# Optimization experiments

Measured on AMD Instinct MI355X. Metric: run time of the kernel, lower is better.

## Reference

```python
import jax, jax.numpy as jnp
import numpy as np

EMBED_DIM = 768
NUM_HEADS = 12
HEAD_DIM = EMBED_DIM // NUM_HEADS
SCALE = HEAD_DIM ** -0.5


def setup_inputs() -> dict:
    key = jax.random.key(0)
    ks = jax.random.split(key, 9)
    B, S, D = 2, 2048, EMBED_DIM
    init = 1.0 / np.sqrt(D)  # ~ nn.Linear default uniform scale
    x = jax.random.normal(ks[0], (B, S, D), dtype=jnp.float32)
    Wq = jax.random.uniform(ks[1], (D, D), jnp.float32, -init, init)
    bq = jax.random.uniform(ks[2], (D,), jnp.float32, -init, init)
    Wk = jax.random.uniform(ks[3], (D, D), jnp.float32, -init, init)
    bk = jax.random.uniform(ks[4], (D,), jnp.float32, -init, init)
    Wv = jax.random.uniform(ks[5], (D, D), jnp.float32, -init, init)
    bv = jax.random.uniform(ks[6], (D,), jnp.float32, -init, init)
    Wo = jax.random.uniform(ks[7], (D, D), jnp.float32, -init, init)
    bo = jax.random.uniform(ks[8], (D,), jnp.float32, -init, init)
    return {"x": x, "Wq": Wq, "bq": bq, "Wk": Wk, "bk": bk,
            "Wv": Wv, "bv": bv, "Wo": Wo, "bo": bo}


def reference(x, Wq, bq, Wk, bk, Wv, bv, Wo, bo):
    B, S, D = x.shape
    H, Dh = NUM_HEADS, HEAD_DIM
    # projections; weights stored as (in, out) so x @ W == torch Linear with W.T
    q = (x @ Wq + bq).reshape(B, S, H, Dh).transpose(0, 2, 1, 3)  # [B,H,S,Dh]
    k = (x @ Wk + bk).reshape(B, S, H, Dh).transpose(0, 2, 1, 3)
    v = (x @ Wv + bv).reshape(B, S, H, Dh).transpose(0, 2, 1, 3)
    scores = jnp.einsum("bhqd,bhkd->bhqk", q, k) * SCALE        # [B,H,S,S]
    weights = jax.nn.softmax(scores, axis=-1)
    out = jnp.einsum("bhqk,bhkd->bhqd", weights, v)              # [B,H,S,Dh]
    out = out.transpose(0, 2, 1, 3).reshape(B, S, D)
    return out @ Wo + bo
```

## Files before the change

kernel.cpp:

```cpp
#include <hip/hip_runtime.h>
#include <math.h>

#define BB 2
#define SS 2048
#define DDIM 768
#define HH 12
#define DH 64
#define NROWS (BB*SS)
#define NTOK_D (NROWS*DDIM)
#define NQT2 (SS/128)

typedef _Float16 f16;
typedef _Float16 half2v __attribute__((ext_vector_type(2)));
typedef __fp16 fp16x2 __attribute__((ext_vector_type(2)));
typedef _Float16 half4 __attribute__((ext_vector_type(4)));
typedef _Float16 half8 __attribute__((ext_vector_type(8)));
typedef float f32x4 __attribute__((ext_vector_type(4)));

__device__ __forceinline__ half2v cvt_pk_f16(float a, float b) {
    fp16x2 t = __builtin_amdgcn_cvt_pkrtz(a, b);
    return __builtin_bit_cast(half2v, t);
}

#define MFMA16(a,b,c) __builtin_amdgcn_mfma_f32_16x16x32_f16((a),(b),(c),0,0,0)
#define QSCALE (0.125f * 1.44269504088896f)
#define M_STATIC 10.0f

__device__ __forceinline__ int swz(int row, int chunk16) {
    return row*128 + ((chunk16 ^ (row & 7)) << 4);
}

__global__ __launch_bounds__(256) void prep_x(const float* __restrict__ x, f16* __restrict__ xh)
{
    int i = blockIdx.x * 256 + threadIdx.x;
    const float4* in = (const float4*)x;
    float4 a = in[i*2], b = in[i*2+1];
    half8 h = {(f16)a.x,(f16)a.y,(f16)a.z,(f16)a.w,(f16)b.x,(f16)b.y,(f16)b.z,(f16)b.w};
    *(half8*)(xh + (size_t)i*8) = h;
}

__global__ __launch_bounds__(256) void prep_w(const float* __restrict__ Wq, const float* __restrict__ Wk,
                                              const float* __restrict__ Wv, const float* __restrict__ Wo,
                                              f16* __restrict__ Wt)
{
    const int z = blockIdx.z;
    const float* W = z==0 ? Wq : (z==1 ? Wk : (z==2 ? Wv : Wo));
    f16* out = Wt + (size_t)z * DDIM * DDIM;

    __shared__ float tile[64][65];
    const int t = threadIdx.x;
    const int k0 = blockIdx.x*64, n0 = blockIdx.y*64;

    const int kr = t >> 2, nc = (t & 3) * 16;
    #pragma unroll
    for (int i = 0; i < 4; ++i) {
        float4 v = *(const float4*)&W[(size_t)(k0+kr)*DDIM + n0 + nc + i*4];
        tile[kr][nc+i*4+0] = v.x; tile[kr][nc+i*4+1] = v.y;
        tile[kr][nc+i*4+2] = v.z; tile[kr][nc+i*4+3] = v.w;
    }
    __syncthreads();
    const int nr = t >> 2, kc = (t & 3) * 16;
    half8 h0, h1;
    #pragma unroll
    for (int j = 0; j < 8; ++j) {
        h0[j] = (f16)tile[kc + j][nr];
        h1[j] = (f16)tile[kc + 8 + j][nr];
    }
    *(half8*)&out[(size_t)(n0+nr)*DDIM + k0 + kc]     = h0;
    *(half8*)&out[(size_t)(n0+nr)*DDIM + k0 + kc + 8] = h1;
}

__global__ __launch_bounds__(256) void proj_qkv(const f16* __restrict__ Xh, const f16* __restrict__ Wt,
        const float* __restrict__ bq, const float* __restrict__ bk, const float* __restrict__ bv,
        f16* __restrict__ qb, f16* __restrict__ kb2, f16* __restrict__ vtb)
{
    const int z = blockIdx.z;
    const f16* Wz = Wt + (size_t)z * DDIM * DDIM;
    const float* bias = z==0 ? bq : (z==1 ? bk : bv);
    const float qscale = (z==0) ? QSCALE : 1.0f;

    __shared__ __align__(16) unsigned char lds[64*1024];

    const int tid = threadIdx.x;
    const int l = tid & 63, w = tid >> 6;
    const int g = l >> 4, qi = l & 15;
    const int wm = w >> 1, wn = w & 1;
    const int m0 = blockIdx.x * 128, n0 = blockIdx.y * 128;

    f32x4 acc[4][4];
    #pragma unroll
    for (int i=0;i<4;i++)
        #pragma unroll
        for (int j=0;j<4;j++) { f32x4 zv = {0.f,0.f,0.f,0.f}; acc[i][j] = zv; }

    half8 sa[4], sb[4];

#define GLOAD(t) { \
        _Pragma("unroll") \
        for (int i = 0; i < 4; ++i) { \
            int c = i*256 + tid, row = c >> 3, kc = c & 7; \
            sa[i] = *(const half8*)&Xh[(size_t)(m0+row)*DDIM + (t)*64 + kc*8]; \
            sb[i] = *(const half8*)&Wz[(size_t)(n0+row)*DDIM + (t)*64 + kc*8]; \
        } }

#define GWRT(bufi) { \
        unsigned char* As_ = lds + (bufi)*32768; \
        unsigned char* Bs_ = As_ + 16384; \
        _Pragma("unroll") \
        for (int i = 0; i < 4; ++i) { \
            int c = i*256 + tid, row = c >> 3, kc = c & 7; \
            *(half8*)(As_ + swz(row, kc)) = sa[i]; \
            *(half8*)(Bs_ + swz(row, kc)) = sb[i]; \
        } }

    GLOAD(0); GWRT(0);
    __syncthreads();

    for (int t = 0; t < 12; ++t) {
        const int cur = t & 1;
        if (t < 11) GLOAD(t+1);

        const unsigned char* As = lds + cur*32768;
        const unsigned char* Bs = As + 16384;

        half8 af[4][2], bf[4][2];
        #pragma unroll
        for (int mt = 0; mt < 4; ++mt) {
            int row = wm*64 + mt*16 + qi;
            #pragma unroll
            for (int kh = 0; kh < 2; ++kh)
                af[mt][kh] = *(const half8*)(As + swz(row, kh*4 + g));
        }
        #pragma unroll
        for (int nt = 0; nt < 4; ++nt) {
            int row = wn*64 + nt*16 + qi;
            #pragma unroll
            for (int kh = 0; kh < 2; ++kh)
                bf[nt][kh] = *(const half8*)(Bs + swz(row, kh*4 + g));
        }
        __builtin_amdgcn_s_setprio(1);
        #pragma unroll
        for (int mt = 0; mt < 4; ++mt)
            #pragma unroll
            for (int nt = 0; nt < 4; ++nt) {
                acc[mt][nt] = MFMA16(af[mt][0], bf[nt][0], acc[mt][nt]);
                acc[mt][nt] = MFMA16(af[mt][1], bf[nt][1], acc[mt][nt]);
            }
        __builtin_amdgcn_s_setprio(0);

        if (t < 11) GWRT(cur^1);
        __syncthreads();
    }

    if (z == 2) {
        #pragma unroll
        for (int mt = 0; mt < 4; ++mt)
            #pragma unroll
            for (int nt = 0; nt < 4; ++nt) {
                int m = m0 + wm*64 + mt*16 + g*4;
                int n = n0 + wn*64 + nt*16 + qi;
                int b = m >> 11, s = m & 2047;
                int h = n >> 6,  d = n & 63;
                float bs = bias[n];
                half4 o4 = {(f16)(acc[mt][nt][0] + bs), (f16)(acc[mt][nt][1] + bs),
                            (f16)(acc[mt][nt][2] + bs), (f16)(acc[mt][nt][3] + bs)};
                *(half4*)&vtb[(((size_t)(b*HH + h))*DH + d)*SS + s] = o4;
            }
    } else {
        f16* out = (z == 0) ? qb : kb2;
        #pragma unroll
        for (int mt = 0; mt < 4; ++mt)
            #pragma unroll
            for (int nt = 0; nt < 4; ++nt)
                #pragma unroll
                for (int r = 0; r < 4; ++r) {
                    int m = m0 + wm*64 + mt*16 + g*4 + r;
                    int n = n0 + wn*64 + nt*16 + qi;
                    float v = (acc[mt][nt][r] + bias[n]) * qscale;
                    int b = m >> 11, s = m & 2047;
                    int h = n >> 6,  d = n & 63;
                    out[(((size_t)(b*HH + h))*SS + s)*DH + d] = (f16)v;
                }
    }
#undef GLOAD
#undef GWRT
}

__global__ __launch_bounds__(256) void attn_mfma(
        const f16* __restrict__ qbuf, const f16* __restrict__ kbuf,
        const f16* __restrict__ vtbuf, f16* __restrict__ pO, float* __restrict__ mlb)
{
    __shared__ __align__(16) unsigned char lds[48*1024];

    const int tid = threadIdx.x;
    const int l = tid & 63, w = tid >> 6;
    const int g = l >> 4, qi = l & 15;
    const int qt = blockIdx.x, h = blockIdx.y;
    const int b = blockIdx.z >> 1, khalf = blockIdx.z & 1;
    const int q0 = qt * 128 + w * 32;
    const size_t base = ((size_t)(b * HH + h)) * SS * DH;
    const int key0 = khalf * (SS/2);
    const int pid = (b * HH + h) * NQT2 + qt;

    unsigned char* Pw = lds + 32768 + w*4096;

    half8 qf[2][2];
    #pragma unroll
    for (int f = 0; f < 2; ++f)
        #pragma unroll
        for (int kh = 0; kh < 2; ++kh)
            qf[f][kh] = *(const half8*)&qbuf[base + (size_t)(q0 + f*16 + qi)*DH + kh*32 + g*8];

    f32x4 oacc[2][4];
    #pragma unroll
    for (int f = 0; f < 2; ++f)
        #pragma unroll
        for (int i = 0; i < 4; ++i) { f32x4 zv = {0.f,0.f,0.f,0.f}; oacc[f][i] = zv; }
    float lsum[2] = {0.f, 0.f};
    const f32x4 minit = {-M_STATIC, -M_STATIC, -M_STATIC, -M_STATIC};

    half8 sk[2], svv[2];

#define LOADT(t) { \
        _Pragma("unroll") \
        for (int i = 0; i < 2; ++i) { \
            int c = i*256 + tid, row = c >> 3, col = c & 7; \
            sk[i]  = *(const half8*)&kbuf[base + (size_t)(key0 + (t)*64 + row)*DH + col*8]; \
            svv[i] = *(const half8*)&vtbuf[base + (size_t)row*SS + key0 + (t)*64 + col*8]; \
        } }

#define WRT(bufi) { \
        unsigned char* Kw_ = lds + (bufi)*16384; \
        unsigned char* Vw_ = Kw_ + 8192; \
        _Pragma("unroll") \
        for (int i = 0; i < 2; ++i) { \
            int c = i*256 + tid, row = c >> 3, col = c & 7; \
            *(half8*)(Kw_ + swz(row, col)) = sk[i]; \
            *(half8*)(Vw_ + swz(row, col)) = svv[i]; \
        } }

    LOADT(0); WRT(0);
    __syncthreads();

    for (int t = 0; t < 16; ++t) {
        const int cur = t & 1;
        if (t < 15) LOADT(t+1);

        const unsigned char* Kb = lds + cur*16384;
        const unsigned char* Vb = Kb + 8192;

        half8 kf[8];
        #pragma unroll
        for (int mt = 0; mt < 4; ++mt)
            #pragma unroll
            for (int kh = 0; kh < 2; ++kh)
                kf[mt*2+kh] = *(const half8*)(Kb + swz(mt*16 + qi, kh*4 + g));
        half8 vf[8];
        #pragma unroll
        for (int dt = 0; dt < 4; ++dt)
            #pragma unroll
            for (int kh = 0; kh < 2; ++kh)
                vf[dt*2+kh] = *(const half8*)(Vb + swz(dt*16 + qi, kh*4 + g));

        #pragma unroll
        for (int f = 0; f < 2; ++f) {
            f32x4 sv[4];
            __builtin_amdgcn_s_setprio(1);
            #pragma unroll
            for (int mt = 0; mt < 4; ++mt) {
                f32x4 zz = MFMA16(kf[mt*2+0], qf[f][0], minit);
                sv[mt] = MFMA16(kf[mt*2+1], qf[f][1], zz);
            }
            __builtin_amdgcn_s_setprio(0);
            half2v ph[8];
            #pragma unroll
            for (int mt = 0; mt < 4; ++mt) {
                float e0 = exp2f(sv[mt][0]);
                float e1 = exp2f(sv[mt][1]);
                float e2 = exp2f(sv[mt][2]);
                float e3 = exp2f(sv[mt][3]);
                ph[mt*2+0] = cvt_pk_f16(e0, e1);
                ph[mt*2+1] = cvt_pk_f16(e2, e3);
                half4 pk = {ph[mt*2+0][0], ph[mt*2+0][1], ph[mt*2+1][0], ph[mt*2+1][1]};
                *(half4*)(Pw + swz(f*16 + qi, 2*mt + (g>>1)) + (g&1)*8) = pk;
            }
            half2v s01 = (ph[0] + ph[1]) + (ph[2] + ph[3]);
            half2v s23 = (ph[4] + ph[5]) + (ph[6] + ph[7]);
            half2v st = s01 + s23;
            float rs = (float)st[0] + (float)st[1];
            rs += __shfl_xor(rs, 16);
            rs += __shfl_xor(rs, 32);
            lsum[f] += rs;
        }

        #pragma unroll
        for (int f = 0; f < 2; ++f) {
            half8 pf0 = *(const half8*)(Pw + swz(f*16 + qi, g));
            half8 pf1 = *(const half8*)(Pw + swz(f*16 + qi, 4 + g));
            __builtin_amdgcn_s_setprio(1);
            #pragma unroll
            for (int dt = 0; dt < 4; ++dt) {
                oacc[f][dt] = MFMA16(vf[dt*2+0], pf0, oacc[f][dt]);
                oacc[f][dt] = MFMA16(vf[dt*2+1], pf1, oacc[f][dt]);
            }
            __builtin_amdgcn_s_setprio(0);
        }

        if (t < 15) WRT(cur^1);
        __syncthreads();
    }

    f16* po = pO + ((size_t)pid*2 + khalf) * (128*64);
    float* mlp = mlb + ((size_t)pid*2 + khalf) * 128;
    #pragma unroll
    for (int f = 0; f < 2; ++f) {
        const int qw = w*32 + f*16 + qi;
        const float inv = 1.0f / lsum[f];
        #pragma unroll
        for (int dt = 0; dt < 4; ++dt) {
            half4 o4 = {(f16)(oacc[f][dt][0]*inv), (f16)(oacc[f][dt][1]*inv),
                        (f16)(oacc[f][dt][2]*inv), (f16)(oacc[f][dt][3]*inv)};
            *(half4*)&po[qw*64 + dt*16 + g*4] = o4;
        }
        if (g == 0) mlp[qw] = lsum[f];
    }
#undef LOADT
#undef WRT
}

__global__ __launch_bounds__(256) void attn_combine(
        const f16* __restrict__ pO, const float* __restrict__ mlb, f16* __restrict__ ob)
{
    const int gr = blockIdx.x*64 + (threadIdx.x >> 2);
    const int dg = (threadIdx.x & 3) << 4;
    const int bh = gr >> 11, s = gr & 2047;
    const int qt = s >> 7, qr = s & 127;
    const int pid = bh * NQT2 + qt;

    const f16* O0 = pO + ((size_t)pid*2 + 0)*(128*64) + qr*64;
    const f16* O1 = pO + ((size_t)pid*2 + 1)*(128*64) + qr*64;
    float l0 = mlb[((size_t)pid*2 + 0)*128 + qr];
    float l1 = mlb[((size_t)pid*2 + 1)*128 + qr];
    float inv = 1.0f / (l0 + l1);
    float w0 = l0 * inv, w1 = l1 * inv;

    half8 x0 = *(const half8*)&O0[dg];
    half8 x1 = *(const half8*)&O0[dg + 8];
    half8 y0 = *(const half8*)&O1[dg];
    half8 y1 = *(const half8*)&O1[dg + 8];
    half8 r0, r1;
    #pragma unroll
    for (int j = 0; j < 8; ++j) {
        r0[j] = (f16)(w0*(float)x0[j] + w1*(float)y0[j]);
        r1[j] = (f16)(w0*(float)x1[j] + w1*(float)y1[j]);
    }
    f16* dst = &ob[((size_t)bh*SS + s)*DH + dg];
    *(half8*)dst = r0;
    *(half8*)(dst + 8) = r1;
}

__global__ __launch_bounds__(256) void proj_out(const f16* __restrict__ obuf, const f16* __restrict__ Wt,
                                                const float* __restrict__ bo, float* __restrict__ out)
{
    const f16* Wz = Wt + (size_t)3 * DDIM * DDIM;

    __shared__ __align__(16) unsigned char lds[64*1024];

    const int tid = threadIdx.x;
    const int l = tid & 63, w = tid >> 6;
    const int g = l >> 4, qi = l & 15;
    const int wm = w >> 1, wn = w & 1;
    const int m0 = blockIdx.x * 128, n0 = blockIdx.y * 128;

    f32x4 acc[4][4];
    #pragma unroll
    for (int i=0;i<4;i++)
        #pragma unroll
        for (int j=0;j<4;j++) { f32x4 zv = {0.f,0.f,0.f,0.f}; acc[i][j] = zv; }

    half8 sa[4], sb[4];

#define GLOAD(t) { \
        _Pragma("unroll") \
        for (int i = 0; i < 4; ++i) { \
            int c = i*256 + tid, row = c >> 3, kc = c & 7; \
            int m = m0 + row, bb_ = m >> 11, ss_ = m & 2047; \
            sa[i] = *(const half8*)&obuf[(((size_t)(bb_*HH + (t)))*SS + ss_)*DH + kc*8]; \
            sb[i] = *(const half8*)&Wz[(size_t)(n0+row)*DDIM + (t)*64 + kc*8]; \
        } }

#define GWRT(bufi) { \
        unsigned char* As_ = lds + (bufi)*32768; \
        unsigned char* Bs_ = As_ + 16384; \
        _Pragma("unroll") \
        for (int i = 0; i < 4; ++i) { \
            int c = i*256 + tid, row = c >> 3, kc = c & 7; \
            *(half8*)(As_ + swz(row, kc)) = sa[i]; \
            *(half8*)(Bs_ + swz(row, kc)) = sb[i]; \
        } }

    GLOAD(0); GWRT(0);
    __syncthreads();

    for (int t = 0; t < 12; ++t) {
        const int cur = t & 1;
        if (t < 11) GLOAD(t+1);

        const unsigned char* As = lds + cur*32768;
        const unsigned char* Bs = As + 16384;

        half8 af[4][2], bf[4][2];
        #pragma unroll
        for (int mt = 0; mt < 4; ++mt) {
            int row = wm*64 + mt*16 + qi;
            #pragma unroll
            for (int kh = 0; kh < 2; ++kh)
                af[mt][kh] = *(const half8*)(As + swz(row, kh*4 + g));
        }
        #pragma unroll
        for (int nt = 0; nt < 4; ++nt) {
            int row = wn*64 + nt*16 + qi;
            #pragma unroll
            for (int kh = 0; kh < 2; ++kh)
                bf[nt][kh] = *(const half8*)(Bs + swz(row, kh*4 + g));
        }
        __builtin_amdgcn_s_setprio(1);
        #pragma unroll
        for (int mt = 0; mt < 4; ++mt)
            #pragma unroll
            for (int nt = 0; nt < 4; ++nt) {
                acc[mt][nt] = MFMA16(af[mt][0], bf[nt][0], acc[mt][nt]);
                acc[mt][nt] = MFMA16(af[mt][1], bf[nt][1], acc[mt][nt]);
            }
        __builtin_amdgcn_s_setprio(0);

        if (t < 11) GWRT(cur^1);
        __syncthreads();
    }

    #pragma unroll
    for (int mt = 0; mt < 4; ++mt)
        #pragma unroll
        for (int nt = 0; nt < 4; ++nt)
            #pragma unroll
            for (int r = 0; r < 4; ++r) {
                int m = m0 + wm*64 + mt*16 + g*4 + r;
                int n = n0 + wn*64 + nt*16 + qi;
                out[(size_t)m*DDIM + n] = acc[mt][nt][r] + bo[n];
            }
#undef GLOAD
#undef GWRT
}

extern "C" void kernel_launch(void* const* d_in, const int* in_sizes, int n_in,
                              void* d_out, int out_size, void* d_ws, size_t ws_size,
                              hipStream_t stream)
{
    const float* x  = (const float*)d_in[0];
    const float* Wq = (const float*)d_in[1];
    const float* bq = (const float*)d_in[2];
    const float* Wk = (const float*)d_in[3];
    const float* bk = (const float*)d_in[4];
    const float* Wv = (const float*)d_in[5];
    const float* bv = (const float*)d_in[6];
    const float* Wo = (const float*)d_in[7];
    const float* bo = (const float*)d_in[8];

    char* ws = (char*)d_ws;
    const size_t XH_B  = (size_t)NTOK_D * 2;
    const size_t WT_B  = (size_t)4 * DDIM * DDIM * 2;
    const size_t HB_B  = (size_t)BB * HH * SS * DH * 2;
    const size_t PO_B  = (size_t)BB * HH * NQT2 * 2 * 128 * 64 * 2;

    f16* Xh = (f16*)ws;
    f16* Wt = (f16*)(ws + XH_B);
    f16* qb = (f16*)(ws + XH_B + WT_B);
    f16* kb = (f16*)(ws + XH_B + WT_B + HB_B);
    f16* vt = (f16*)(ws + XH_B + WT_B + 2*HB_B);
    f16* ob = (f16*)(ws + XH_B + WT_B + 3*HB_B);
    f16* pO = (f16*)(ws + XH_B + WT_B + 4*HB_B);
    float* mlb = (float*)(ws + XH_B + WT_B + 4*HB_B + PO_B);

    prep_x<<<NTOK_D/(256*8), 256, 0, stream>>>(x, Xh);
    prep_w<<<dim3(DDIM/64, DDIM/64, 4), 256, 0, stream>>>(Wq, Wk, Wv, Wo, Wt);
    proj_qkv<<<dim3(NROWS/128, DDIM/128, 3), 256, 0, stream>>>(Xh, Wt, bq, bk, bv, qb, kb, vt);
    attn_mfma<<<dim3(NQT2, HH, BB*2), 256, 0, stream>>>(qb, kb, vt, pO, mlb);
    attn_combine<<<dim3(BB*HH*SS/64), 256, 0, stream>>>(pO, mlb, ob);
    proj_out<<<dim3(NROWS/128, DDIM/128), 256, 0, stream>>>(ob, Wt, bo, (float*)d_out);
}
```

Measured before the change: 118.5 us.

## Fuse x fp16 conversion into QKV GEMM and split-K combine into out-projection

Removes the prep_x kernel by having proj_qkv load fp32 x directly and convert to fp16 while staging tiles. Removes attn_combine by having proj_out read both split-KV partial outputs and their row sums and merge them while loading its A tile. This drops two launches and the intermediate buffers' write and read traffic. The cost is redundant work: x is re-read and re-converted once per N-tile and per projection, and the partials are re-merged by every N-block of the out projection, which also doubles A-side global reads there.

```diff
diff --git a/kernel.cpp b/kernel.cpp
--- a/kernel.cpp
+++ b/kernel.cpp
@@ -7,7 +7,6 @@
 #define HH 12
 #define DH 64
 #define NROWS (BB*SS)
-#define NTOK_D (NROWS*DDIM)
 #define NQT2 (SS/128)
 
 typedef _Float16 f16;
@@ -28,15 +27,6 @@
 
 __device__ __forceinline__ int swz(int row, int chunk16) {
     return row*128 + ((chunk16 ^ (row & 7)) << 4);
-}
-
-__global__ __launch_bounds__(256) void prep_x(const float* __restrict__ x, f16* __restrict__ xh)
-{
-    int i = blockIdx.x * 256 + threadIdx.x;
-    const float4* in = (const float4*)x;
-    float4 a = in[i*2], b = in[i*2+1];
-    half8 h = {(f16)a.x,(f16)a.y,(f16)a.z,(f16)a.w,(f16)b.x,(f16)b.y,(f16)b.z,(f16)b.w};
-    *(half8*)(xh + (size_t)i*8) = h;
 }
 
 __global__ __launch_bounds__(256) void prep_w(const float* __restrict__ Wq, const float* __restrict__ Wk,
@@ -70,7 +60,7 @@
     *(half8*)&out[(size_t)(n0+nr)*DDIM + k0 + kc + 8] = h1;
 }
 
-__global__ __launch_bounds__(256) void proj_qkv(const f16* __restrict__ Xh, const f16* __restrict__ Wt,
+__global__ __launch_bounds__(256) void proj_qkv(const float* __restrict__ x, const f16* __restrict__ Wt,
         const float* __restrict__ bq, const float* __restrict__ bk, const float* __restrict__ bv,
         f16* __restrict__ qb, f16* __restrict__ kb2, f16* __restrict__ vtb)
 {
@@ -99,7 +89,12 @@
         _Pragma("unroll") \
         for (int i = 0; i < 4; ++i) { \
             int c = i*256 + tid, row = c >> 3, kc = c & 7; \
-            sa[i] = *(const half8*)&Xh[(size_t)(m0+row)*DDIM + (t)*64 + kc*8]; \
+            const float* xp = &x[(size_t)(m0+row)*DDIM + (t)*64 + kc*8]; \
+            float4 a0 = *(const float4*)xp; \
+            float4 a1 = *(const float4*)(xp + 4); \
+            half8 hv = {(f16)a0.x,(f16)a0.y,(f16)a0.z,(f16)a0.w, \
+                        (f16)a1.x,(f16)a1.y,(f16)a1.z,(f16)a1.w}; \
+            sa[i] = hv; \
             sb[i] = *(const half8*)&Wz[(size_t)(n0+row)*DDIM + (t)*64 + kc*8]; \
         } }
 
@@ -328,39 +323,9 @@
 #undef WRT
 }
 
-__global__ __launch_bounds__(256) void attn_combine(
-        const f16* __restrict__ pO, const float* __restrict__ mlb, f16* __restrict__ ob)
-{
-    const int gr = blockIdx.x*64 + (threadIdx.x >> 2);
-    const int dg = (threadIdx.x & 3) << 4;
-    const int bh = gr >> 11, s = gr & 2047;
-    const int qt = s >> 7, qr = s & 127;
-    const int pid = bh * NQT2 + qt;
-
-    const f16* O0 = pO + ((size_t)pid*2 + 0)*(128*64) + qr*64;
-    const f16* O1 = pO + ((size_t)pid*2 + 1)*(128*64) + qr*64;
-    float l0 = mlb[((size_t)pid*2 + 0)*128 + qr];
-    float l1 = mlb[((size_t)pid*2 + 1)*128 + qr];
-    float inv = 1.0f / (l0 + l1);
-    float w0 = l0 * inv, w1 = l1 * inv;
-
-    half8 x0 = *(const half8*)&O0[dg];
-    half8 x1 = *(const half8*)&O0[dg + 8];
-    half8 y0 = *(const half8*)&O1[dg];
-    half8 y1 = *(const half8*)&O1[dg + 8];
-    half8 r0, r1;
-    #pragma unroll
-    for (int j = 0; j < 8; ++j) {
-        r0[j] = (f16)(w0*(float)x0[j] + w1*(float)y0[j]);
-        r1[j] = (f16)(w0*(float)x1[j] + w1*(float)y1[j]);
-    }
-    f16* dst = &ob[((size_t)bh*SS + s)*DH + dg];
-    *(half8*)dst = r0;
-    *(half8*)(dst + 8) = r1;
-}
-
-__global__ __launch_bounds__(256) void proj_out(const f16* __restrict__ obuf, const f16* __restrict__ Wt,
-                                                const float* __restrict__ bo, float* __restrict__ out)
+__global__ __launch_bounds__(256) void proj_out(const f16* __restrict__ pO, const float* __restrict__ mlb,
+                                                const f16* __restrict__ Wt, const float* __restrict__ bo,
+                                                float* __restrict__ out)
 {
     const f16* Wz = Wt + (size_t)3 * DDIM * DDIM;
 
@@ -385,7 +350,21 @@
         for (int i = 0; i < 4; ++i) { \
             int c = i*256 + tid, row = c >> 3, kc = c & 7; \
             int m = m0 + row, bb_ = m >> 11, ss_ = m & 2047; \
-            sa[i] = *(const half8*)&obuf[(((size_t)(bb_*HH + (t)))*SS + ss_)*DH + kc*8]; \
+            int qt_ = ss_ >> 7, qr_ = ss_ & 127; \
+            int pid_ = (bb_*HH + (t))*NQT2 + qt_; \
+            const f16* P0_ = pO + ((size_t)pid_*2 + 0)*(128*64) + qr_*64 + kc*8; \
+            const f16* P1_ = pO + ((size_t)pid_*2 + 1)*(128*64) + qr_*64 + kc*8; \
+            half8 xv = *(const half8*)P0_; \
+            half8 yv = *(const half8*)P1_; \
+            float l0 = mlb[((size_t)pid_*2 + 0)*128 + qr_]; \
+            float l1 = mlb[((size_t)pid_*2 + 1)*128 + qr_]; \
+            float winv = 1.0f / (l0 + l1); \
+            float w0 = l0 * winv, w1 = l1 * winv; \
+            half8 rv; \
+            _Pragma("unroll") \
+            for (int j = 0; j < 8; ++j) \
+                rv[j] = (f16)(w0*(float)xv[j] + w1*(float)yv[j]); \
+            sa[i] = rv; \
             sb[i] = *(const half8*)&Wz[(size_t)(n0+row)*DDIM + (t)*64 + kc*8]; \
         } }
 
@@ -467,24 +446,19 @@
     const float* bo = (const float*)d_in[8];
 
     char* ws = (char*)d_ws;
-    const size_t XH_B  = (size_t)NTOK_D * 2;
     const size_t WT_B  = (size_t)4 * DDIM * DDIM * 2;
     const size_t HB_B  = (size_t)BB * HH * SS * DH * 2;
     const size_t PO_B  = (size_t)BB * HH * NQT2 * 2 * 128 * 64 * 2;
 
-    f16* Xh = (f16*)ws;
-    f16* Wt = (f16*)(ws + XH_B);
-    f16* qb = (f16*)(ws + XH_B + WT_B);
-    f16* kb = (f16*)(ws + XH_B + WT_B + HB_B);
-    f16* vt = (f16*)(ws + XH_B + WT_B + 2*HB_B);
-    f16* ob = (f16*)(ws + XH_B + WT_B + 3*HB_B);
-    f16* pO = (f16*)(ws + XH_B + WT_B + 4*HB_B);
-    float* mlb = (float*)(ws + XH_B + WT_B + 4*HB_B + PO_B);
-
-    prep_x<<<NTOK_D/(256*8), 256, 0, stream>>>(x, Xh);
+    f16* Wt = (f16*)ws;
+    f16* qb = (f16*)(ws + WT_B);
+    f16* kb = (f16*)(ws + WT_B + HB_B);
+    f16* vt = (f16*)(ws + WT_B + 2*HB_B);
+    f16* pO = (f16*)(ws + WT_B + 3*HB_B);
+    float* mlb = (float*)(ws + WT_B + 3*HB_B + PO_B);
+
     prep_w<<<dim3(DDIM/64, DDIM/64, 4), 256, 0, stream>>>(Wq, Wk, Wv, Wo, Wt);
-    proj_qkv<<<dim3(NROWS/128, DDIM/128, 3), 256, 0, stream>>>(Xh, Wt, bq, bk, bv, qb, kb, vt);
+    proj_qkv<<<dim3(NROWS/128, DDIM/128, 3), 256, 0, stream>>>(x, Wt, bq, bk, bv, qb, kb, vt);
     attn_mfma<<<dim3(NQT2, HH, BB*2), 256, 0, stream>>>(qb, kb, vt, pO, mlb);
-    attn_combine<<<dim3(BB*HH*SS/64), 256, 0, stream>>>(pO, mlb, ob);
-    proj_out<<<dim3(NROWS/128, DDIM/128), 256, 0, stream>>>(ob, Wt, bo, (float*)d_out);
-}
+    proj_out<<<dim3(NROWS/128, DDIM/128), 256, 0, stream>>>(pO, mlb, Wt, bo, (float*)d_out);
+}
```

Measured after the change: 120.3 us. No clear change (+1.5%).
